# Optimization experiments

Measured on AMD Instinct MI355X. Metric: run time of the kernel, lower is better.

The kernel has to match this reference:

```python
import jax, jax.numpy as jnp
import numpy as np

B, S, H = 4, 2048, 2048
I, E, K = 1408, 16, 2


def setup_inputs() -> dict:
    key = jax.random.key(0)
    ks = jax.random.split(key, 8)
    sc = 0.02  # init scale for weights
    return {
        "hidden_states": jax.random.normal(ks[0], (B, S, H), jnp.float32),
        "gate_w": jax.random.normal(ks[1], (E, H), jnp.float32) * sc,
        "bias": jnp.zeros((E,), jnp.float32),
        "shared_w1": jax.random.normal(ks[2], (I, H), jnp.float32) * sc,
        "shared_w3": jax.random.normal(ks[3], (I, H), jnp.float32) * sc,
        "shared_w2": jax.random.normal(ks[4], (H, I), jnp.float32) * sc,
        "w1": jax.random.normal(ks[5], (E, I, H), jnp.float32) * sc,
        "w3": jax.random.normal(ks[6], (E, I, H), jnp.float32) * sc,
        "w2": jax.random.normal(ks[7], (E, H, I), jnp.float32) * sc,
    }


def _swiglu(x, a, b, c):
    # torch Linear convention: weight [out, in] -> x @ W.T
    return (jax.nn.silu(x @ a.T) * (x @ b.T)) @ c.T


def reference(hidden_states, gate_w, bias, shared_w1, shared_w3, shared_w2, w1, w3, w2):
    orig_shape = hidden_states.shape
    x = hidden_states.reshape(-1, orig_shape[-1])  # [T, H]
    T = x.shape[0]

    # shared expert (num_shared_experts = 1)
    shared_output = _swiglu(x, shared_w1, shared_w3, shared_w2)

    # sigmoid-gated top-k routing with bias-corrected selection
    logits = x @ gate_w.T                       # [T, E]
    scores = jax.nn.sigmoid(logits)
    routing_scores = scores + bias
    _, topk_idx = jax.lax.top_k(routing_scores, K)          # [T, K]
    sel = jnp.take_along_axis(scores, topk_idx, axis=1)     # gate on raw scores
    gating = sel / sel.sum(axis=-1, keepdims=True)          # [T, K]

    # dense combine matrix [T, E]: gating value where selected, else 0
    combine = jnp.zeros((T, E), x.dtype).at[jnp.arange(T)[:, None], topk_idx].add(gating)

    # per-expert SwiGLU, weighted combine (loop over fixed small E)
    routed_output = jnp.zeros_like(x)
    for e in range(E):
        y = _swiglu(x, w1[e], w3[e], w2[e])     # [T, H]
        routed_output = routed_output + combine[:, e:e + 1] * y

    return (shared_output + routed_output).reshape(orig_shape)
```

## Files before the change

### kernel.cpp

```cpp
#include <hip/hip_runtime.h>
#include <hip/hip_bf16.h>
#include <stdint.h>

#define T_TOK 8192
#define H_DIM 2048
#define I_DIM 1408
#define E_NUM 16

typedef __hip_bfloat16 bf16;
typedef __bf16 bf16x8 __attribute__((ext_vector_type(8)));
typedef float f32x4 __attribute__((ext_vector_type(4)));

#define M_CNT 0
#define M_OFF 16
#define M_CUR 33
#define M_WLC 49
#define M_WLE 64
#define M_WLM 224

#define GLOAD_LDS16(g, l)                                                          \
  __builtin_amdgcn_global_load_lds(                                               \
      (const __attribute__((address_space(1))) void*)(g),                         \
      (__attribute__((address_space(3))) void*)(l), 16, 0, 0)

__global__ void zero_meta_kernel(int* __restrict__ meta) {
  for (int i = threadIdx.x; i < 1024; i += 256) meta[i] = 0;
}

__global__ void cvt_kernel(const float* __restrict__ src, bf16* __restrict__ dst, long n) {
  long i = ((long)blockIdx.x * 256 + threadIdx.x) * 4;
  const long stride = (long)gridDim.x * 256 * 4;
  for (; i < n; i += stride) {
    const float4 v = *reinterpret_cast<const float4*>(src + i);
    union { bf16 b[4]; ushort4 u; } o;
    o.b[0] = __float2bfloat16(v.x);
    o.b[1] = __float2bfloat16(v.y);
    o.b[2] = __float2bfloat16(v.z);
    o.b[3] = __float2bfloat16(v.w);
    *reinterpret_cast<ushort4*>(dst + i) = o.u;
  }
}

__global__ __launch_bounds__(256) void gate_kernel(
    const float* __restrict__ X, const float* __restrict__ GW,
    const float* __restrict__ bias, int* __restrict__ topk_idx,
    float* __restrict__ topk_gate, int* __restrict__ meta) {
  const int lane = threadIdx.x & 63;
  const int t = blockIdx.x * 4 + (threadIdx.x >> 6);
  const float* xr = X + (size_t)t * H_DIM;
  float acc[E_NUM];
#pragma unroll
  for (int e = 0; e < E_NUM; ++e) acc[e] = 0.f;
  for (int h = lane; h < H_DIM; h += 64) {
    const float xv = xr[h];
#pragma unroll
    for (int e = 0; e < E_NUM; ++e) acc[e] += xv * GW[e * H_DIM + h];
  }
#pragma unroll
  for (int o = 32; o > 0; o >>= 1) {
#pragma unroll
    for (int e = 0; e < E_NUM; ++e) acc[e] += __shfl_xor(acc[e], o);
  }
  if (lane == 0) {
    float s[E_NUM], r[E_NUM];
#pragma unroll
    for (int e = 0; e < E_NUM; ++e) {
      s[e] = 1.f / (1.f + expf(-acc[e]));
      r[e] = s[e] + bias[e];
    }
    int i1 = 0;
    for (int e = 1; e < E_NUM; ++e) if (r[e] > r[i1]) i1 = e;
    int i2 = (i1 == 0) ? 1 : 0;
    for (int e = 0; e < E_NUM; ++e) if (e != i1 && r[e] > r[i2]) i2 = e;
    const float g1 = s[i1], g2 = s[i2];
    const float inv = 1.f / (g1 + g2);
    topk_idx[2 * t] = i1;
    topk_idx[2 * t + 1] = i2;
    topk_gate[2 * t] = g1 * inv;
    topk_gate[2 * t + 1] = g2 * inv;
    atomicAdd(&meta[M_CNT + i1], 1);
    atomicAdd(&meta[M_CNT + i2], 1);
  }
}

__global__ void scan_kernel(int* __restrict__ meta) {
  if (threadIdx.x == 0) {
    int off = 0, nw = 0;
    for (int e = 0; e < E_NUM; ++e) {
      meta[M_OFF + e] = off;
      const int c = meta[M_CNT + e];
      const int nt = (c + 127) >> 7;
      for (int i = 0; i < nt; ++i) { meta[M_WLE + nw] = e; meta[M_WLM + nw] = i; ++nw; }
      off += c;
      meta[M_CUR + e] = 0;
    }
    meta[M_OFF + 16] = off;
    meta[M_WLC] = nw;
  }
}

__global__ void scatter_kernel(const int* __restrict__ topk_idx,
                               const float* __restrict__ topk_gate,
                               int* __restrict__ meta, int* __restrict__ list_token,
                               float* __restrict__ list_gate) {
  const int t = blockIdx.x * 256 + threadIdx.x;
#pragma unroll
  for (int k = 0; k < 2; ++k) {
    const int e = topk_idx[2 * t + k];
    const float g = topk_gate[2 * t + k];
    const int slot = atomicAdd(&meta[M_CUR + e], 1);
    const int p = meta[M_OFF + e] + slot;
    list_token[p] = t;
    list_gate[p] = g;
  }
}

template <bool ROUTED>
__global__ __launch_bounds__(256, 2) void gemm1_dual_kernel(
    const bf16* __restrict__ X, const bf16* __restrict__ W1,
    const bf16* __restrict__ W3, bf16* __restrict__ Hout,
    const int* __restrict__ meta, const int* __restrict__ list_token,
    const float* __restrict__ list_gate) {
  __shared__ alignas(16) bf16 As[128 * 32];
  __shared__ alignas(16) bf16 B1s[128 * 32];
  __shared__ alignas(16) bf16 B3s[128 * 32];

  const int tid = threadIdx.x;
  const int lane = tid & 63;
  const int wid = tid >> 6;

  int mt, nt, nrows = T_TOK, rowbase = 0;
  const bf16 *w1p, *w3p;
  if constexpr (ROUTED) {
    if ((int)blockIdx.x >= meta[M_WLC]) return;
    const int e = meta[M_WLE + blockIdx.x];
    mt = meta[M_WLM + blockIdx.x];
    nt = blockIdx.y;
    rowbase = meta[M_OFF + e];
    nrows = meta[M_CNT + e];
    w1p = W1 + (size_t)e * I_DIM * H_DIM;
    w3p = W3 + (size_t)e * I_DIM * H_DIM;
  } else {
    mt = blockIdx.x;
    nt = blockIdx.y;
    w1p = W1;
    w3p = W3;
  }

  const int r0 = tid >> 2, r1 = (tid + 256) >> 2;
  const int kc0 = (tid & 3) * 8, kc1 = ((tid + 256) & 3) * 8;
  long arow0, arow1;
  if constexpr (ROUTED) {
    int s0 = mt * 128 + r0; if (s0 > nrows - 1) s0 = nrows - 1;
    int s1 = mt * 128 + r1; if (s1 > nrows - 1) s1 = nrows - 1;
    arow0 = list_token[rowbase + s0];
    arow1 = list_token[rowbase + s1];
  } else {
    arow0 = (long)mt * 128 + r0;
    arow1 = (long)mt * 128 + r1;
  }
  const long brow0 = (long)nt * 128 + r0;
  const long brow1 = (long)nt * 128 + r1;

  const bf16* ap0 = X + (size_t)arow0 * H_DIM + kc0;
  const bf16* ap1 = X + (size_t)arow1 * H_DIM + kc1;
  const bf16* b1p0 = w1p + (size_t)brow0 * H_DIM + kc0;
  const bf16* b1p1 = w1p + (size_t)brow1 * H_DIM + kc1;
  const bf16* b3p0 = w3p + (size_t)brow0 * H_DIM + kc0;
  const bf16* b3p1 = w3p + (size_t)brow1 * H_DIM + kc1;

  bf16* As_w0 = As + wid * 512;
  bf16* As_w1 = As + 2048 + wid * 512;
  bf16* B1_w0 = B1s + wid * 512;
  bf16* B1_w1 = B1s + 2048 + wid * 512;
  bf16* B3_w0 = B3s + wid * 512;
  bf16* B3_w1 = B3s + 2048 + wid * 512;

  f32x4 acc1[4][4], acc3[4][4];
#pragma unroll
  for (int i = 0; i < 4; ++i)
#pragma unroll
    for (int j = 0; j < 4; ++j) {
      acc1[i][j] = (f32x4){0.f, 0.f, 0.f, 0.f};
      acc3[i][j] = (f32x4){0.f, 0.f, 0.f, 0.f};
    }

  const int wm = wid >> 1, wn = wid & 1;
  const int fr = lane & 15;
  const int kof = (lane >> 4) * 8;

  for (int kt = 0; kt < H_DIM / 32; ++kt) {
    const int k0 = kt * 32;
    GLOAD_LDS16(ap0 + k0, As_w0);
    GLOAD_LDS16(ap1 + k0, As_w1);
    GLOAD_LDS16(b1p0 + k0, B1_w0);
    GLOAD_LDS16(b1p1 + k0, B1_w1);
    GLOAD_LDS16(b3p0 + k0, B3_w0);
    GLOAD_LDS16(b3p1 + k0, B3_w1);
    __syncthreads();

    bf16x8 a[4], b1[4], b3[4];
#pragma unroll
    for (int mf = 0; mf < 4; ++mf)
      a[mf] = *reinterpret_cast<const bf16x8*>(&As[(wm * 64 + mf * 16 + fr) * 32 + kof]);
#pragma unroll
    for (int nf = 0; nf < 4; ++nf) {
      b1[nf] = *reinterpret_cast<const bf16x8*>(&B1s[(wn * 64 + nf * 16 + fr) * 32 + kof]);
      b3[nf] = *reinterpret_cast<const bf16x8*>(&B3s[(wn * 64 + nf * 16 + fr) * 32 + kof]);
    }
#pragma unroll
    for (int mf = 0; mf < 4; ++mf)
#pragma unroll
      for (int nf = 0; nf < 4; ++nf) {
        acc1[mf][nf] = __builtin_amdgcn_mfma_f32_16x16x32_bf16(a[mf], b1[nf], acc1[mf][nf], 0, 0, 0);
        acc3[mf][nf] = __builtin_amdgcn_mfma_f32_16x16x32_bf16(a[mf], b3[nf], acc3[mf][nf], 0, 0, 0);
      }
    __syncthreads();
  }

#pragma unroll
  for (int mf = 0; mf < 4; ++mf)
#pragma unroll
    for (int nf = 0; nf < 4; ++nf)
#pragma unroll
      for (int j = 0; j < 4; ++j) {
        const int rl = wm * 64 + mf * 16 + (lane >> 4) * 4 + j;
        const int col = nt * 128 + wn * 64 + nf * 16 + fr;
        const float z = acc1[mf][nf][j];
        float h = z / (1.f + expf(-z)) * acc3[mf][nf][j];
        if constexpr (ROUTED) {
          const int slot = mt * 128 + rl;
          if (slot < nrows) {
            h *= list_gate[rowbase + slot];
            Hout[(size_t)(rowbase + slot) * I_DIM + col] = __float2bfloat16(h);
          }
        } else {
          Hout[(size_t)(mt * 128 + rl) * I_DIM + col] = __float2bfloat16(h);
        }
      }
}

template <bool ROUTED>
__global__ __launch_bounds__(256, 2) void gemm2_kernel(
    const bf16* __restrict__ Hin, const bf16* __restrict__ W2,
    float* __restrict__ Out, const int* __restrict__ meta,
    const int* __restrict__ list_token) {
  __shared__ alignas(16) bf16 As[128 * 32];
  __shared__ alignas(16) bf16 Bs[128 * 32];

  const int tid = threadIdx.x;
  const int lane = tid & 63;
  const int wid = tid >> 6;

  int mt, nt, nrows = T_TOK, rowbase = 0;
  const bf16* w2p;
  if constexpr (ROUTED) {
    if ((int)blockIdx.x >= meta[M_WLC]) return;
    const int e = meta[M_WLE + blockIdx.x];
    mt = meta[M_WLM + blockIdx.x];
    nt = blockIdx.y;
    rowbase = meta[M_OFF + e];
    nrows = meta[M_CNT + e];
    w2p = W2 + (size_t)e * H_DIM * I_DIM;
  } else {
    mt = blockIdx.x;
    nt = blockIdx.y;
    w2p = W2;
  }

  const int r0 = tid >> 2, r1 = (tid + 256) >> 2;
  const int kc0 = (tid & 3) * 8, kc1 = ((tid + 256) & 3) * 8;
  const long arow0 = (long)rowbase + mt * 128 + r0;
  const long arow1 = (long)rowbase + mt * 128 + r1;
  const long brow0 = (long)nt * 128 + r0;
  const long brow1 = (long)nt * 128 + r1;

  const bf16* ap0 = Hin + (size_t)arow0 * I_DIM + kc0;
  const bf16* ap1 = Hin + (size_t)arow1 * I_DIM + kc1;
  const bf16* bp0 = w2p + (size_t)brow0 * I_DIM + kc0;
  const bf16* bp1 = w2p + (size_t)brow1 * I_DIM + kc1;

  bf16* As_w0 = As + wid * 512;
  bf16* As_w1 = As + 2048 + wid * 512;
  bf16* Bs_w0 = Bs + wid * 512;
  bf16* Bs_w1 = Bs + 2048 + wid * 512;

  f32x4 acc[4][4];
#pragma unroll
  for (int i = 0; i < 4; ++i)
#pragma unroll
    for (int j = 0; j < 4; ++j) acc[i][j] = (f32x4){0.f, 0.f, 0.f, 0.f};

  const int wm = wid >> 1, wn = wid & 1;
  const int fr = lane & 15;
  const int kof = (lane >> 4) * 8;

  for (int kt = 0; kt < I_DIM / 32; ++kt) {
    const int k0 = kt * 32;
    GLOAD_LDS16(ap0 + k0, As_w0);
    GLOAD_LDS16(ap1 + k0, As_w1);
    GLOAD_LDS16(bp0 + k0, Bs_w0);
    GLOAD_LDS16(bp1 + k0, Bs_w1);
    __syncthreads();

    bf16x8 a[4], b[4];
#pragma unroll
    for (int mf = 0; mf < 4; ++mf)
      a[mf] = *reinterpret_cast<const bf16x8*>(&As[(wm * 64 + mf * 16 + fr) * 32 + kof]);
#pragma unroll
    for (int nf = 0; nf < 4; ++nf)
      b[nf] = *reinterpret_cast<const bf16x8*>(&Bs[(wn * 64 + nf * 16 + fr) * 32 + kof]);
#pragma unroll
    for (int mf = 0; mf < 4; ++mf)
#pragma unroll
      for (int nf = 0; nf < 4; ++nf)
        acc[mf][nf] = __builtin_amdgcn_mfma_f32_16x16x32_bf16(a[mf], b[nf], acc[mf][nf], 0, 0, 0);
    __syncthreads();
  }

#pragma unroll
  for (int mf = 0; mf < 4; ++mf)
#pragma unroll
    for (int nf = 0; nf < 4; ++nf)
#pragma unroll
      for (int j = 0; j < 4; ++j) {
        const int rl = wm * 64 + mf * 16 + (lane >> 4) * 4 + j;
        const int col = nt * 128 + wn * 64 + nf * 16 + fr;
        const float v = acc[mf][nf][j];
        if constexpr (ROUTED) {
          const int slot = mt * 128 + rl;
          if (slot < nrows) {
            const int tok = list_token[rowbase + slot];
            atomicAdd(&Out[(size_t)tok * H_DIM + col], v);
          }
        } else {
          Out[(size_t)(mt * 128 + rl) * H_DIM + col] = v;
        }
      }
}

extern "C" void kernel_launch(void* const* d_in, const int* in_sizes, int n_in,
                              void* d_out, int out_size, void* d_ws, size_t ws_size,
                              hipStream_t stream) {
  const float* x_f = (const float*)d_in[0];
  const float* gw_f = (const float*)d_in[1];
  const float* bias_f = (const float*)d_in[2];
  const float* sw1_f = (const float*)d_in[3];
  const float* sw3_f = (const float*)d_in[4];
  const float* sw2_f = (const float*)d_in[5];
  const float* w1_f = (const float*)d_in[6];
  const float* w3_f = (const float*)d_in[7];
  const float* w2_f = (const float*)d_in[8];
  float* out = (float*)d_out;

  char* ws = (char*)d_ws;
  size_t off = 0;
  auto alloc = [&](size_t bytes) {
    char* p = ws + off;
    off += (bytes + 255) & ~(size_t)255;
    return p;
  };

  bf16* x_bf = (bf16*)alloc((size_t)T_TOK * H_DIM * 2);
  bf16* sw1_bf = (bf16*)alloc((size_t)I_DIM * H_DIM * 2);
  bf16* sw3_bf = (bf16*)alloc((size_t)I_DIM * H_DIM * 2);
  bf16* sw2_bf = (bf16*)alloc((size_t)H_DIM * I_DIM * 2);
  bf16* w1_bf = (bf16*)alloc((size_t)E_NUM * I_DIM * H_DIM * 2);
  bf16* w3_bf = (bf16*)alloc((size_t)E_NUM * I_DIM * H_DIM * 2);
  bf16* w2_bf = (bf16*)alloc((size_t)E_NUM * H_DIM * I_DIM * 2);
  bf16* h_sh = (bf16*)alloc((size_t)T_TOK * I_DIM * 2);
  bf16* h_rt = (bf16*)alloc((size_t)(2 * T_TOK + 256) * I_DIM * 2);
  int* meta = (int*)alloc(4096);
  int* topk_idx = (int*)alloc((size_t)T_TOK * 2 * 4);
  float* topk_gate = (float*)alloc((size_t)T_TOK * 2 * 4);
  int* list_token = (int*)alloc((size_t)T_TOK * 2 * 4);
  float* list_gate = (float*)alloc((size_t)T_TOK * 2 * 4);

  if (off > ws_size) return;

  zero_meta_kernel<<<1, 256, 0, stream>>>(meta);

  auto cvt = [&](const float* s, bf16* d, long n) {
    int blocks = (int)((n / 4 + 255) / 256);
    if (blocks > 8192) blocks = 8192;
    cvt_kernel<<<blocks, 256, 0, stream>>>(s, d, n);
  };
  cvt(x_f, x_bf, (long)T_TOK * H_DIM);
  cvt(sw1_f, sw1_bf, (long)I_DIM * H_DIM);
  cvt(sw3_f, sw3_bf, (long)I_DIM * H_DIM);
  cvt(sw2_f, sw2_bf, (long)H_DIM * I_DIM);
  cvt(w1_f, w1_bf, (long)E_NUM * I_DIM * H_DIM);
  cvt(w3_f, w3_bf, (long)E_NUM * I_DIM * H_DIM);
  cvt(w2_f, w2_bf, (long)E_NUM * H_DIM * I_DIM);

  gate_kernel<<<T_TOK / 4, 256, 0, stream>>>(x_f, gw_f, bias_f, topk_idx, topk_gate, meta);
  scan_kernel<<<1, 64, 0, stream>>>(meta);
  scatter_kernel<<<T_TOK / 256, 256, 0, stream>>>(topk_idx, topk_gate, meta, list_token, list_gate);

  gemm1_dual_kernel<false><<<dim3(64, I_DIM / 128), 256, 0, stream>>>(
      x_bf, sw1_bf, sw3_bf, h_sh, meta, nullptr, nullptr);
  gemm2_kernel<false><<<dim3(64, H_DIM / 128), 256, 0, stream>>>(
      h_sh, sw2_bf, out, meta, nullptr);

  gemm1_dual_kernel<true><<<dim3(160, I_DIM / 128), 256, 0, stream>>>(
      x_bf, w1_bf, w3_bf, h_rt, meta, list_token, list_gate);
  gemm2_kernel<true><<<dim3(160, H_DIM / 128), 256, 0, stream>>>(
      h_rt, w2_bf, out, meta, list_token);
}
```

Before: 1.720 ms.

## Merge shared and routed GEMM1 into one launch with balanced worklist, swizzled BK=64 tiles, pre-gathered tokens

Pre-gathers routed token rows into a contiguous buffer so the routed GEMMs load plain strided A tiles. The shared and routed SwiGLU first GEMMs are merged into a single launch driven by a worklist. Each work item covers up to two M-tiles, and items are assigned to slots by a greedy load balancer over sorted expert sizes. The K tile grows from 32 to 64 with an XOR-swizzled LDS layout to reduce bank conflicts. This trades an extra gather pass, more LDS per block and a more complex scheduler for fewer launches, better load balance and fewer barriers per K.

```diff
diff --git a/kernel.cpp b/kernel.cpp
--- a/kernel.cpp
+++ b/kernel.cpp
@@ -6,6 +6,10 @@
 #define H_DIM 2048
 #define I_DIM 1408
 #define E_NUM 16
+#define NT1 11
+#define NT2 16
+#define WLTAB 576
+#define GX_WL 577
 
 typedef __hip_bfloat16 bf16;
 typedef __bf16 bf16x8 __attribute__((ext_vector_type(8)));
@@ -14,17 +18,30 @@
 #define M_CNT 0
 #define M_OFF 16
 #define M_CUR 33
-#define M_WLC 49
-#define M_WLE 64
-#define M_WLM 224
+#define WL1_E 64
+#define WL1_M0 640
+#define WL1_MC 1216
+#define WL2_E 1792
+#define WL2_M0 2368
+#define WL2_MC 2944
+#define META_INTS 3520
 
 #define GLOAD_LDS16(g, l)                                                          \
   __builtin_amdgcn_global_load_lds(                                               \
       (const __attribute__((address_space(1))) void*)(g),                         \
       (__attribute__((address_space(3))) void*)(l), 16, 0, 0)
 
+__device__ __forceinline__ int lds_off(int row, int cc) {
+  return row * 64 + ((cc ^ (row & 7)) * 8);
+}
+
 __global__ void zero_meta_kernel(int* __restrict__ meta) {
-  for (int i = threadIdx.x; i < 1024; i += 256) meta[i] = 0;
+  const int t = threadIdx.x;
+  for (int i = t; i < 64; i += 256) meta[i] = 0;
+  for (int i = t; i < WLTAB; i += 256) {
+    meta[WL1_E + i] = -1;
+    meta[WL2_E + i] = -1;
+  }
 }
 
 __global__ void cvt_kernel(const float* __restrict__ src, bf16* __restrict__ dst, long n) {
@@ -84,18 +101,77 @@
 }
 
 __global__ void scan_kernel(int* __restrict__ meta) {
-  if (threadIdx.x == 0) {
-    int off = 0, nw = 0;
-    for (int e = 0; e < E_NUM; ++e) {
-      meta[M_OFF + e] = off;
-      const int c = meta[M_CNT + e];
-      const int nt = (c + 127) >> 7;
-      for (int i = 0; i < nt; ++i) { meta[M_WLE + nw] = e; meta[M_WLM + nw] = i; ++nw; }
-      off += c;
-      meta[M_CUR + e] = 0;
+  if (threadIdx.x != 0) return;
+  int mt[17];
+  int off = 0;
+  for (int e = 0; e < E_NUM; ++e) {
+    meta[M_OFF + e] = off;
+    const int c = meta[M_CNT + e];
+    off += c;
+    meta[M_CUR + e] = 0;
+    mt[e] = (c + 127) >> 7;
+  }
+  meta[M_OFF + 16] = off;
+  mt[16] = T_TOK / 128;
+
+  int ord[E_NUM];
+  for (int i = 0; i < E_NUM; ++i) ord[i] = i;
+  for (int i = 1; i < E_NUM; ++i) {
+    const int v = ord[i];
+    int j = i;
+    while (j > 0 && mt[ord[j - 1]] < mt[v]) { ord[j] = ord[j - 1]; --j; }
+    ord[j] = v;
+  }
+
+  {
+    int load[8] = {0}, slots[8] = {0};
+    for (int i = 0; i < E_NUM; ++i) {
+      const int e = ord[i];
+      if (mt[e] == 0) continue;
+      int r = 0;
+      for (int k = 1; k < 8; ++k) if (load[k] < load[r]) r = k;
+      for (int c = 0; c < mt[e]; c += 2) {
+        const int wx = slots[r] * 8 + r;
+        ++slots[r];
+        if (wx < WLTAB) {
+          meta[WL1_E + wx] = e;
+          meta[WL1_M0 + wx] = c;
+          meta[WL1_MC + wx] = (mt[e] - c >= 2) ? 2 : 1;
+        }
+      }
+      load[r] += mt[e];
     }
-    meta[M_OFF + 16] = off;
-    meta[M_WLC] = nw;
+    for (int c = 0; c < 64; c += 2) {
+      int r = 0;
+      for (int k = 1; k < 8; ++k) if (load[k] < load[r]) r = k;
+      const int wx = slots[r] * 8 + r;
+      ++slots[r];
+      if (wx < WLTAB) {
+        meta[WL1_E + wx] = 16;
+        meta[WL1_M0 + wx] = c;
+        meta[WL1_MC + wx] = 2;
+      }
+      load[r] += 2;
+    }
+  }
+  {
+    int load[8] = {0}, slots[8] = {0};
+    for (int i = 0; i < E_NUM; ++i) {
+      const int e = ord[i];
+      if (mt[e] == 0) continue;
+      int r = 0;
+      for (int k = 1; k < 8; ++k) if (load[k] < load[r]) r = k;
+      for (int c = 0; c < mt[e]; c += 2) {
+        const int wx = slots[r] * 8 + r;
+        ++slots[r];
+        if (wx < WLTAB) {
+          meta[WL2_E + wx] = e;
+          meta[WL2_M0 + wx] = c;
+          meta[WL2_MC + wx] = (mt[e] - c >= 2) ? 2 : 1;
+        }
+      }
+      load[r] += mt[e];
+    }
   }
 }
 
@@ -115,228 +191,250 @@
   }
 }
 
-template <bool ROUTED>
-__global__ __launch_bounds__(256, 2) void gemm1_dual_kernel(
-    const bf16* __restrict__ X, const bf16* __restrict__ W1,
-    const bf16* __restrict__ W3, bf16* __restrict__ Hout,
-    const int* __restrict__ meta, const int* __restrict__ list_token,
+__global__ void gather_kernel(const bf16* __restrict__ Xb, const int* __restrict__ list_token,
+                              bf16* __restrict__ Xg) {
+  const int lane = threadIdx.x & 63;
+  const int s = blockIdx.x * 4 + (threadIdx.x >> 6);
+  int src = list_token[(s < 2 * T_TOK) ? s : (2 * T_TOK - 1)];
+  const ushort4* in = reinterpret_cast<const ushort4*>(Xb + (size_t)src * H_DIM);
+  ushort4* outp = reinterpret_cast<ushort4*>(Xg + (size_t)s * H_DIM);
+#pragma unroll
+  for (int i = 0; i < H_DIM / 4 / 64; ++i) outp[lane + i * 64] = in[lane + i * 64];
+}
+
+__global__ __launch_bounds__(256, 2) void gemm1_kernel(
+    const bf16* __restrict__ Xg, const bf16* __restrict__ Xs,
+    const bf16* __restrict__ W1, const bf16* __restrict__ W3,
+    const bf16* __restrict__ SW1, const bf16* __restrict__ SW3,
+    bf16* __restrict__ Hout, const int* __restrict__ meta,
     const float* __restrict__ list_gate) {
-  __shared__ alignas(16) bf16 As[128 * 32];
-  __shared__ alignas(16) bf16 B1s[128 * 32];
-  __shared__ alignas(16) bf16 B3s[128 * 32];
+  __shared__ alignas(16) bf16 As[128 * 64];
+  __shared__ alignas(16) bf16 B1s[128 * 64];
+  __shared__ alignas(16) bf16 B3s[128 * 64];
+
+  const int wx = blockIdx.x;
+  if (wx >= WLTAB) return;
+  const int e = meta[WL1_E + wx];
+  if (e < 0) return;
+  const int m0 = meta[WL1_M0 + wx];
+  const int mc = meta[WL1_MC + wx];
+  const int nt = blockIdx.y;
 
   const int tid = threadIdx.x;
   const int lane = tid & 63;
   const int wid = tid >> 6;
 
-  int mt, nt, nrows = T_TOK, rowbase = 0;
-  const bf16 *w1p, *w3p;
-  if constexpr (ROUTED) {
-    if ((int)blockIdx.x >= meta[M_WLC]) return;
-    const int e = meta[M_WLE + blockIdx.x];
-    mt = meta[M_WLM + blockIdx.x];
-    nt = blockIdx.y;
+  const bf16 *abase, *w1p, *w3p;
+  int hbase, nrows, goff;
+  if (e == 16) {
+    abase = Xs; w1p = SW1; w3p = SW3;
+    hbase = 2 * T_TOK; nrows = T_TOK; goff = 0;
+  } else {
+    goff = meta[M_OFF + e];
+    abase = Xg + (size_t)goff * H_DIM;
+    w1p = W1 + (size_t)e * I_DIM * H_DIM;
+    w3p = W3 + (size_t)e * I_DIM * H_DIM;
+    hbase = goff; nrows = meta[M_CNT + e];
+  }
+
+  int srow[4];
+  size_t aoff[4], boff[4];
+#pragma unroll
+  for (int i = 0; i < 4; ++i) {
+    const int c = tid + 256 * i;
+    const int r = c >> 3;
+    const int gc = ((c & 7) ^ (r & 7)) * 8;
+    srow[i] = r;
+    aoff[i] = (size_t)r * H_DIM + gc;
+    boff[i] = (size_t)(nt * 128 + r) * H_DIM + gc;
+  }
+
+  const int wm = wid >> 1, wn = wid & 1;
+  const int fr = lane & 15;
+  const int kg = lane >> 4;
+
+  for (int m = 0; m < mc; ++m) {
+    const bf16* am = abase + (size_t)(m0 + m) * 128 * H_DIM;
+
+    f32x4 acc1[4][4], acc3[4][4];
+#pragma unroll
+    for (int i = 0; i < 4; ++i)
+#pragma unroll
+      for (int j = 0; j < 4; ++j) {
+        acc1[i][j] = (f32x4){0.f, 0.f, 0.f, 0.f};
+        acc3[i][j] = (f32x4){0.f, 0.f, 0.f, 0.f};
+      }
+
+    for (int kt = 0; kt < H_DIM / 64; ++kt) {
+      const int col = kt * 64;
+#pragma unroll
+      for (int i = 0; i < 4; ++i) {
+        bf16* ldst = As + 2048 * i + 512 * wid;
+        GLOAD_LDS16(am + aoff[i] + col, ldst);
+      }
+#pragma unroll
+      for (int i = 0; i < 4; ++i) {
+        bf16* ldst = B1s + 2048 * i + 512 * wid;
+        GLOAD_LDS16(w1p + boff[i] + col, ldst);
+      }
+#pragma unroll
+      for (int i = 0; i < 4; ++i) {
+        bf16* ldst = B3s + 2048 * i + 512 * wid;
+        GLOAD_LDS16(w3p + boff[i] + col, ldst);
+      }
+      __syncthreads();
+
+#pragma unroll
+      for (int ks = 0; ks < 2; ++ks) {
+        bf16x8 a[4], b1[4], b3[4];
+        const int cc = 4 * ks + kg;
+#pragma unroll
+        for (int mf = 0; mf < 4; ++mf)
+          a[mf] = *reinterpret_cast<const bf16x8*>(&As[lds_off(wm * 64 + mf * 16 + fr, cc)]);
+#pragma unroll
+        for (int nf = 0; nf < 4; ++nf) {
+          b1[nf] = *reinterpret_cast<const bf16x8*>(&B1s[lds_off(wn * 64 + nf * 16 + fr, cc)]);
+          b3[nf] = *reinterpret_cast<const bf16x8*>(&B3s[lds_off(wn * 64 + nf * 16 + fr, cc)]);
+        }
+#pragma unroll
+        for (int mf = 0; mf < 4; ++mf)
+#pragma unroll
+          for (int nf = 0; nf < 4; ++nf) {
+            acc1[mf][nf] = __builtin_amdgcn_mfma_f32_16x16x32_bf16(a[mf], b1[nf], acc1[mf][nf], 0, 0, 0);
+            acc3[mf][nf] = __builtin_amdgcn_mfma_f32_16x16x32_bf16(a[mf], b3[nf], acc3[mf][nf], 0, 0, 0);
+          }
+      }
+      __syncthreads();
+    }
+
+#pragma unroll
+    for (int mf = 0; mf < 4; ++mf)
+#pragma unroll
+      for (int nf = 0; nf < 4; ++nf)
+#pragma unroll
+        for (int j = 0; j < 4; ++j) {
+          const int rl = wm * 64 + mf * 16 + (lane >> 4) * 4 + j;
+          const int srel = (m0 + m) * 128 + rl;
+          if (srel < nrows) {
+            const int col = nt * 128 + wn * 64 + nf * 16 + fr;
+            const float z = acc1[mf][nf][j];
+            float h = z / (1.f + expf(-z)) * acc3[mf][nf][j];
+            if (e != 16) h *= list_gate[goff + srel];
+            Hout[(size_t)(hbase + srel) * I_DIM + col] = __float2bfloat16(h);
+          }
+        }
+  }
+}
+
+template <bool SHARED>
+__global__ __launch_bounds__(256, 2) void gemm2_kernel(
+    const bf16* __restrict__ Hin, const bf16* __restrict__ W2,
+    const bf16* __restrict__ SW2, float* __restrict__ Out,
+    const int* __restrict__ meta, const int* __restrict__ list_token) {
+  __shared__ alignas(16) bf16 As[128 * 64];
+  __shared__ alignas(16) bf16 Bs[128 * 64];
+
+  int e = 0, m0, mc, nrows, rowbase;
+  const bf16* w2p;
+  if constexpr (SHARED) {
+    m0 = blockIdx.x; mc = 1;
+    nrows = T_TOK; rowbase = 2 * T_TOK;
+    w2p = SW2;
+  } else {
+    const int wx = blockIdx.x;
+    if (wx >= WLTAB) return;
+    e = meta[WL2_E + wx];
+    if (e < 0) return;
+    m0 = meta[WL2_M0 + wx];
+    mc = meta[WL2_MC + wx];
     rowbase = meta[M_OFF + e];
     nrows = meta[M_CNT + e];
-    w1p = W1 + (size_t)e * I_DIM * H_DIM;
-    w3p = W3 + (size_t)e * I_DIM * H_DIM;
-  } else {
-    mt = blockIdx.x;
-    nt = blockIdx.y;
-    w1p = W1;
-    w3p = W3;
-  }
-
-  const int r0 = tid >> 2, r1 = (tid + 256) >> 2;
-  const int kc0 = (tid & 3) * 8, kc1 = ((tid + 256) & 3) * 8;
-  long arow0, arow1;
-  if constexpr (ROUTED) {
-    int s0 = mt * 128 + r0; if (s0 > nrows - 1) s0 = nrows - 1;
-    int s1 = mt * 128 + r1; if (s1 > nrows - 1) s1 = nrows - 1;
-    arow0 = list_token[rowbase + s0];
-    arow1 = list_token[rowbase + s1];
-  } else {
-    arow0 = (long)mt * 128 + r0;
-    arow1 = (long)mt * 128 + r1;
-  }
-  const long brow0 = (long)nt * 128 + r0;
-  const long brow1 = (long)nt * 128 + r1;
-
-  const bf16* ap0 = X + (size_t)arow0 * H_DIM + kc0;
-  const bf16* ap1 = X + (size_t)arow1 * H_DIM + kc1;
-  const bf16* b1p0 = w1p + (size_t)brow0 * H_DIM + kc0;
-  const bf16* b1p1 = w1p + (size_t)brow1 * H_DIM + kc1;
-  const bf16* b3p0 = w3p + (size_t)brow0 * H_DIM + kc0;
-  const bf16* b3p1 = w3p + (size_t)brow1 * H_DIM + kc1;
-
-  bf16* As_w0 = As + wid * 512;
-  bf16* As_w1 = As + 2048 + wid * 512;
-  bf16* B1_w0 = B1s + wid * 512;
-  bf16* B1_w1 = B1s + 2048 + wid * 512;
-  bf16* B3_w0 = B3s + wid * 512;
-  bf16* B3_w1 = B3s + 2048 + wid * 512;
-
-  f32x4 acc1[4][4], acc3[4][4];
-#pragma unroll
-  for (int i = 0; i < 4; ++i)
-#pragma unroll
-    for (int j = 0; j < 4; ++j) {
-      acc1[i][j] = (f32x4){0.f, 0.f, 0.f, 0.f};
-      acc3[i][j] = (f32x4){0.f, 0.f, 0.f, 0.f};
-    }
-
-  const int wm = wid >> 1, wn = wid & 1;
-  const int fr = lane & 15;
-  const int kof = (lane >> 4) * 8;
-
-  for (int kt = 0; kt < H_DIM / 32; ++kt) {
-    const int k0 = kt * 32;
-    GLOAD_LDS16(ap0 + k0, As_w0);
-    GLOAD_LDS16(ap1 + k0, As_w1);
-    GLOAD_LDS16(b1p0 + k0, B1_w0);
-    GLOAD_LDS16(b1p1 + k0, B1_w1);
-    GLOAD_LDS16(b3p0 + k0, B3_w0);
-    GLOAD_LDS16(b3p1 + k0, B3_w1);
-    __syncthreads();
-
-    bf16x8 a[4], b1[4], b3[4];
-#pragma unroll
-    for (int mf = 0; mf < 4; ++mf)
-      a[mf] = *reinterpret_cast<const bf16x8*>(&As[(wm * 64 + mf * 16 + fr) * 32 + kof]);
-#pragma unroll
-    for (int nf = 0; nf < 4; ++nf) {
-      b1[nf] = *reinterpret_cast<const bf16x8*>(&B1s[(wn * 64 + nf * 16 + fr) * 32 + kof]);
-      b3[nf] = *reinterpret_cast<const bf16x8*>(&B3s[(wn * 64 + nf * 16 + fr) * 32 + kof]);
-    }
-#pragma unroll
-    for (int mf = 0; mf < 4; ++mf)
-#pragma unroll
-      for (int nf = 0; nf < 4; ++nf) {
-        acc1[mf][nf] = __builtin_amdgcn_mfma_f32_16x16x32_bf16(a[mf], b1[nf], acc1[mf][nf], 0, 0, 0);
-        acc3[mf][nf] = __builtin_amdgcn_mfma_f32_16x16x32_bf16(a[mf], b3[nf], acc3[mf][nf], 0, 0, 0);
-      }
-    __syncthreads();
-  }
-
-#pragma unroll
-  for (int mf = 0; mf < 4; ++mf)
-#pragma unroll
-    for (int nf = 0; nf < 4; ++nf)
-#pragma unroll
-      for (int j = 0; j < 4; ++j) {
-        const int rl = wm * 64 + mf * 16 + (lane >> 4) * 4 + j;
-        const int col = nt * 128 + wn * 64 + nf * 16 + fr;
-        const float z = acc1[mf][nf][j];
-        float h = z / (1.f + expf(-z)) * acc3[mf][nf][j];
-        if constexpr (ROUTED) {
-          const int slot = mt * 128 + rl;
-          if (slot < nrows) {
-            h *= list_gate[rowbase + slot];
-            Hout[(size_t)(rowbase + slot) * I_DIM + col] = __float2bfloat16(h);
-          }
-        } else {
-          Hout[(size_t)(mt * 128 + rl) * I_DIM + col] = __float2bfloat16(h);
-        }
-      }
-}
-
-template <bool ROUTED>
-__global__ __launch_bounds__(256, 2) void gemm2_kernel(
-    const bf16* __restrict__ Hin, const bf16* __restrict__ W2,
-    float* __restrict__ Out, const int* __restrict__ meta,
-    const int* __restrict__ list_token) {
-  __shared__ alignas(16) bf16 As[128 * 32];
-  __shared__ alignas(16) bf16 Bs[128 * 32];
+    w2p = W2 + (size_t)e * H_DIM * I_DIM;
+  }
+  const int nt = blockIdx.y;
 
   const int tid = threadIdx.x;
   const int lane = tid & 63;
   const int wid = tid >> 6;
 
-  int mt, nt, nrows = T_TOK, rowbase = 0;
-  const bf16* w2p;
-  if constexpr (ROUTED) {
-    if ((int)blockIdx.x >= meta[M_WLC]) return;
-    const int e = meta[M_WLE + blockIdx.x];
-    mt = meta[M_WLM + blockIdx.x];
-    nt = blockIdx.y;
-    rowbase = meta[M_OFF + e];
-    nrows = meta[M_CNT + e];
-    w2p = W2 + (size_t)e * H_DIM * I_DIM;
-  } else {
-    mt = blockIdx.x;
-    nt = blockIdx.y;
-    w2p = W2;
-  }
-
-  const int r0 = tid >> 2, r1 = (tid + 256) >> 2;
-  const int kc0 = (tid & 3) * 8, kc1 = ((tid + 256) & 3) * 8;
-  const long arow0 = (long)rowbase + mt * 128 + r0;
-  const long arow1 = (long)rowbase + mt * 128 + r1;
-  const long brow0 = (long)nt * 128 + r0;
-  const long brow1 = (long)nt * 128 + r1;
-
-  const bf16* ap0 = Hin + (size_t)arow0 * I_DIM + kc0;
-  const bf16* ap1 = Hin + (size_t)arow1 * I_DIM + kc1;
-  const bf16* bp0 = w2p + (size_t)brow0 * I_DIM + kc0;
-  const bf16* bp1 = w2p + (size_t)brow1 * I_DIM + kc1;
-
-  bf16* As_w0 = As + wid * 512;
-  bf16* As_w1 = As + 2048 + wid * 512;
-  bf16* Bs_w0 = Bs + wid * 512;
-  bf16* Bs_w1 = Bs + 2048 + wid * 512;
-
-  f32x4 acc[4][4];
-#pragma unroll
-  for (int i = 0; i < 4; ++i)
-#pragma unroll
-    for (int j = 0; j < 4; ++j) acc[i][j] = (f32x4){0.f, 0.f, 0.f, 0.f};
+  int srow[4];
+  size_t aoff[4], boff[4];
+#pragma unroll
+  for (int i = 0; i < 4; ++i) {
+    const int c = tid + 256 * i;
+    const int r = c >> 3;
+    const int gc = ((c & 7) ^ (r & 7)) * 8;
+    srow[i] = r;
+    aoff[i] = (size_t)r * I_DIM + gc;
+    boff[i] = (size_t)(nt * 128 + r) * I_DIM + gc;
+  }
 
   const int wm = wid >> 1, wn = wid & 1;
   const int fr = lane & 15;
-  const int kof = (lane >> 4) * 8;
-
-  for (int kt = 0; kt < I_DIM / 32; ++kt) {
-    const int k0 = kt * 32;
-    GLOAD_LDS16(ap0 + k0, As_w0);
-    GLOAD_LDS16(ap1 + k0, As_w1);
-    GLOAD_LDS16(bp0 + k0, Bs_w0);
-    GLOAD_LDS16(bp1 + k0, Bs_w1);
-    __syncthreads();
-
-    bf16x8 a[4], b[4];
+  const int kg = lane >> 4;
+
+  for (int m = 0; m < mc; ++m) {
+    const bf16* am = Hin + ((size_t)rowbase + (size_t)(m0 + m) * 128) * I_DIM;
+
+    f32x4 acc[4][4];
+#pragma unroll
+    for (int i = 0; i < 4; ++i)
+#pragma unroll
+      for (int j = 0; j < 4; ++j) acc[i][j] = (f32x4){0.f, 0.f, 0.f, 0.f};
+
+    for (int kt = 0; kt < I_DIM / 64; ++kt) {
+      const int col = kt * 64;
+#pragma unroll
+      for (int i = 0; i < 4; ++i) {
+        bf16* ldst = As + 2048 * i + 512 * wid;
+        GLOAD_LDS16(am + aoff[i] + col, ldst);
+      }
+#pragma unroll
+      for (int i = 0; i < 4; ++i) {
+        bf16* ldst = Bs + 2048 * i + 512 * wid;
+        GLOAD_LDS16(w2p + boff[i] + col, ldst);
+      }
+      __syncthreads();
+
+#pragma unroll
+      for (int ks = 0; ks < 2; ++ks) {
+        bf16x8 a[4], b[4];
+        const int cc = 4 * ks + kg;
+#pragma unroll
+        for (int mf = 0; mf < 4; ++mf)
+          a[mf] = *reinterpret_cast<const bf16x8*>(&As[lds_off(wm * 64 + mf * 16 + fr, cc)]);
+#pragma unroll
+        for (int nf = 0; nf < 4; ++nf)
+          b[nf] = *reinterpret_cast<const bf16x8*>(&Bs[lds_off(wn * 64 + nf * 16 + fr, cc)]);
+#pragma unroll
+        for (int mf = 0; mf < 4; ++mf)
+#pragma unroll
+          for (int nf = 0; nf < 4; ++nf)
+            acc[mf][nf] = __builtin_amdgcn_mfma_f32_16x16x32_bf16(a[mf], b[nf], acc[mf][nf], 0, 0, 0);
+      }
+      __syncthreads();
+    }
+
 #pragma unroll
     for (int mf = 0; mf < 4; ++mf)
-      a[mf] = *reinterpret_cast<const bf16x8*>(&As[(wm * 64 + mf * 16 + fr) * 32 + kof]);
-#pragma unroll
-    for (int nf = 0; nf < 4; ++nf)
-      b[nf] = *reinterpret_cast<const bf16x8*>(&Bs[(wn * 64 + nf * 16 + fr) * 32 + kof]);
-#pragma unroll
-    for (int mf = 0; mf < 4; ++mf)
 #pragma unroll
       for (int nf = 0; nf < 4; ++nf)
-        acc[mf][nf] = __builtin_amdgcn_mfma_f32_16x16x32_bf16(a[mf], b[nf], acc[mf][nf], 0, 0, 0);
-    __syncthreads();
-  }
-
-#pragma unroll
-  for (int mf = 0; mf < 4; ++mf)
-#pragma unroll
-    for (int nf = 0; nf < 4; ++nf)
-#pragma unroll
-      for (int j = 0; j < 4; ++j) {
-        const int rl = wm * 64 + mf * 16 + (lane >> 4) * 4 + j;
-        const int col = nt * 128 + wn * 64 + nf * 16 + fr;
-        const float v = acc[mf][nf][j];
-        if constexpr (ROUTED) {
-          const int slot = mt * 128 + rl;
-          if (slot < nrows) {
-            const int tok = list_token[rowbase + slot];
-            atomicAdd(&Out[(size_t)tok * H_DIM + col], v);
+#pragma unroll
+        for (int j = 0; j < 4; ++j) {
+          const int rl = wm * 64 + mf * 16 + (lane >> 4) * 4 + j;
+          const int srel = (m0 + m) * 128 + rl;
+          const int col = nt * 128 + wn * 64 + nf * 16 + fr;
+          const float v = acc[mf][nf][j];
+          if constexpr (SHARED) {
+            Out[(size_t)srel * H_DIM + col] = v;
+          } else {
+            if (srel < nrows) {
+              const int tok = list_token[rowbase + srel];
+              atomicAdd(&Out[(size_t)tok * H_DIM + col], v);
+            }
           }
-        } else {
-          Out[(size_t)(mt * 128 + rl) * H_DIM + col] = v;
         }
-      }
+  }
 }
 
 extern "C" void kernel_launch(void* const* d_in, const int* in_sizes, int n_in,
@@ -362,15 +460,15 @@
   };
 
   bf16* x_bf = (bf16*)alloc((size_t)T_TOK * H_DIM * 2);
+  bf16* xg = (bf16*)alloc((size_t)(2 * T_TOK + 128) * H_DIM * 2);
   bf16* sw1_bf = (bf16*)alloc((size_t)I_DIM * H_DIM * 2);
   bf16* sw3_bf = (bf16*)alloc((size_t)I_DIM * H_DIM * 2);
   bf16* sw2_bf = (bf16*)alloc((size_t)H_DIM * I_DIM * 2);
   bf16* w1_bf = (bf16*)alloc((size_t)E_NUM * I_DIM * H_DIM * 2);
   bf16* w3_bf = (bf16*)alloc((size_t)E_NUM * I_DIM * H_DIM * 2);
   bf16* w2_bf = (bf16*)alloc((size_t)E_NUM * H_DIM * I_DIM * 2);
-  bf16* h_sh = (bf16*)alloc((size_t)T_TOK * I_DIM * 2);
-  bf16* h_rt = (bf16*)alloc((size_t)(2 * T_TOK + 256) * I_DIM * 2);
-  int* meta = (int*)alloc(4096);
+  bf16* h_all = (bf16*)alloc((size_t)(3 * T_TOK + 128) * I_DIM * 2);
+  int* meta = (int*)alloc(META_INTS * 4);
   int* topk_idx = (int*)alloc((size_t)T_TOK * 2 * 4);
   float* topk_gate = (float*)alloc((size_t)T_TOK * 2 * 4);
   int* list_token = (int*)alloc((size_t)T_TOK * 2 * 4);
@@ -396,14 +494,13 @@
   gate_kernel<<<T_TOK / 4, 256, 0, stream>>>(x_f, gw_f, bias_f, topk_idx, topk_gate, meta);
   scan_kernel<<<1, 64, 0, stream>>>(meta);
   scatter_kernel<<<T_TOK / 256, 256, 0, stream>>>(topk_idx, topk_gate, meta, list_token, list_gate);
-
-  gemm1_dual_kernel<false><<<dim3(64, I_DIM / 128), 256, 0, stream>>>(
-      x_bf, sw1_bf, sw3_bf, h_sh, meta, nullptr, nullptr);
-  gemm2_kernel<false><<<dim3(64, H_DIM / 128), 256, 0, stream>>>(
-      h_sh, sw2_bf, out, meta, nullptr);
-
-  gemm1_dual_kernel<true><<<dim3(160, I_DIM / 128), 256, 0, stream>>>(
-      x_bf, w1_bf, w3_bf, h_rt, meta, list_token, list_gate);
-  gemm2_kernel<true><<<dim3(160, H_DIM / 128), 256, 0, stream>>>(
-      h_rt, w2_bf, out, meta, list_token);
-}
+  gather_kernel<<<(2 * T_TOK + 128) / 4, 256, 0, stream>>>(x_bf, list_token, xg);
+
+  gemm1_kernel<<<dim3(GX_WL, NT1), 256, 0, stream>>>(
+      xg, x_bf, w1_bf, w3_bf, sw1_bf, sw3_bf, h_all, meta, list_gate);
+
+  gemm2_kernel<true><<<dim3(T_TOK / 128, NT2), 256, 0, stream>>>(
+      h_all, w2_bf, sw2_bf, out, meta, list_token);
+  gemm2_kernel<false><<<dim3(GX_WL, NT2), 256, 0, stream>>>(
+      h_all, w2_bf, sw2_bf, out, meta, list_token);
+}
```

New measurement: 1.824 ms. +6.1%, slower.
